# Kernel optimization log

Measured on AMD Instinct MI355X. Metric: run time of the kernel, lower is better.

The kernel has to match this reference:

```python
import jax, jax.numpy as jnp
import numpy as np

N, E, D, H, C = 100000, 1600000, 64, 64, 16


def setup_inputs() -> dict:
    key = jax.random.key(0)
    ks = jax.random.split(key, 8)
    x = jax.random.normal(ks[0], (N, D), dtype=jnp.float32)
    edge_index = jax.random.randint(ks[1], (2, E), 0, N, dtype=jnp.int64)
    W1 = jax.random.normal(ks[2], (D, H), dtype=jnp.float32) * (1.0 / np.sqrt(D))
    b1 = jax.random.normal(ks[3], (H,), dtype=jnp.float32) * 0.01
    W2 = jax.random.normal(ks[4], (H, H), dtype=jnp.float32) * (1.0 / np.sqrt(H))
    b2 = jax.random.normal(ks[5], (H,), dtype=jnp.float32) * 0.01
    Wl = jax.random.normal(ks[6], (H, C), dtype=jnp.float32) * (1.0 / np.sqrt(H))
    bl = jax.random.normal(ks[7], (C,), dtype=jnp.float32) * 0.01
    return {"x": x, "edge_index": edge_index, "W1": W1, "b1": b1,
            "W2": W2, "b2": b2, "Wl": Wl, "bl": bl}


def reference(x, edge_index, W1, b1, W2, b2, Wl, bl):
    n = x.shape[0]
    src, dst = edge_index[0], edge_index[1]
    # GCN symmetric normalization with self-loops: deg = 1 + in-degree at dst
    deg = jax.ops.segment_sum(jnp.ones(src.shape[0], x.dtype), dst, num_segments=n) + 1.0
    inv = jax.lax.rsqrt(deg)                      # deg^{-1/2}, [N]
    norm_e = inv[src] * inv[dst]                  # per-edge norm, [E]
    self_w = inv * inv                            # self-loop weight deg^{-1}, [N]

    def gcn(h, W, b):
        h = h @ W                                 # linear transform first (PyG GCNConv)
        agg = jax.ops.segment_sum(h[src] * norm_e[:, None], dst, num_segments=n)
        agg = agg + h * self_w[:, None]           # self-loop contribution
        return agg + b

    h = jax.nn.relu(gcn(x, W1, b1))
    h = jax.nn.relu(gcn(h, W2, b2))
    return h @ Wl + bl
```

## Files before the change

kernel.cpp:

```cpp
#include <hip/hip_runtime.h>
#include <hip/hip_fp16.h>


#define WS_ALIGN 256
#define BSHIFT 8
#define MAXBUCK 512

typedef _Float16 half8 __attribute__((ext_vector_type(8)));
typedef float floatx4 __attribute__((ext_vector_type(4)));


__global__ void k_bhist(const int* __restrict__ dst, int* __restrict__ bhist,
                        int e, int nbuck) {
    __shared__ int hist[MAXBUCK];
    const int CH = 4096;
    int base = blockIdx.x * CH;
    int end = base + CH; if (end > e) end = e;
    for (int t = threadIdx.x; t < nbuck; t += blockDim.x) hist[t] = 0;
    __syncthreads();
    for (int i = base + threadIdx.x; i < end; i += blockDim.x)
        atomicAdd(&hist[dst[i] >> BSHIFT], 1);
    __syncthreads();
    for (int t = threadIdx.x; t < nbuck; t += blockDim.x)
        if (hist[t]) atomicAdd(&bhist[t], hist[t]);
}

__global__ void k_bscan(const int* __restrict__ bhist, int* __restrict__ gbase,
                        int* __restrict__ gcursor, int e, int nbuck) {
    __shared__ int tmp[MAXBUCK];
    int t = threadIdx.x;
    int v = (t < nbuck) ? bhist[t] : 0;
    tmp[t] = v;
    __syncthreads();
    int x = v;
    #pragma unroll
    for (int d = 1; d < MAXBUCK; d <<= 1) {
        int y = (t >= d) ? tmp[t - d] : 0;
        __syncthreads();
        x += y;
        tmp[t] = x;
        __syncthreads();
    }
    if (t < nbuck) { gbase[t] = x - v; gcursor[t] = x - v; }
    if (t == 0) gbase[nbuck] = e;
}

__global__ void k_partition(const int* __restrict__ src, const int* __restrict__ dst,
                            int* __restrict__ gcursor, int* __restrict__ bpairs,
                            int e, int nbuck) {
    __shared__ int hist[MAXBUCK];
    __shared__ int lbase[MAXBUCK];
    const int CH = 4096;
    int base = blockIdx.x * CH;
    int end = base + CH; if (end > e) end = e;
    for (int t = threadIdx.x; t < nbuck; t += blockDim.x) hist[t] = 0;
    __syncthreads();
    for (int i = base + threadIdx.x; i < end; i += blockDim.x)
        atomicAdd(&hist[dst[i] >> BSHIFT], 1);
    __syncthreads();
    for (int t = threadIdx.x; t < nbuck; t += blockDim.x) {
        int c = hist[t];
        lbase[t] = (c > 0) ? atomicAdd(&gcursor[t], c) : 0;
        hist[t] = 0;
    }
    __syncthreads();
    for (int i = base + threadIdx.x; i < end; i += blockDim.x) {
        int s = src[i], d = dst[i];
        int b = d >> BSHIFT;
        int p = lbase[b] + atomicAdd(&hist[b], 1);
        bpairs[p] = (s << BSHIFT) | (d & ((1 << BSHIFT) - 1));
    }
}

__global__ void k_bfin(const int* __restrict__ bpairs, const int* __restrict__ gbase,
                       int2* __restrict__ ocnt, float* __restrict__ inv,
                       int* __restrict__ ssrc, int n) {
    __shared__ int lcnt[256];
    __shared__ int tmp[256];
    __shared__ int loff[256];
    __shared__ int lcur[256];
    const int b = blockIdx.x;
    const int t = threadIdx.x;
    const int lo = gbase[b];
    const int hi = gbase[b + 1];
    lcnt[t] = 0; lcur[t] = 0;
    __syncthreads();
    for (int i = lo + t; i < hi; i += 256)
        atomicAdd(&lcnt[bpairs[i] & 255], 1);
    __syncthreads();
    int v = lcnt[t];
    tmp[t] = v;
    __syncthreads();
    int x = v;
    #pragma unroll
    for (int d = 1; d < 256; d <<= 1) {
        int y = (t >= d) ? tmp[t - d] : 0;
        __syncthreads();
        x += y;
        tmp[t] = x;
        __syncthreads();
    }
    loff[t] = x - v;
    int node = (b << BSHIFT) + t;
    if (node < n) {
        ocnt[node] = make_int2(lo + (x - v), v);
        inv[node] = rsqrtf((float)v + 1.0f);
    }
    __syncthreads();
    for (int i = lo + t; i < hi; i += 256) {
        int p = bpairs[i];
        int l = p & 255;
        int pos = lo + loff[l] + atomicAdd(&lcur[l], 1);
        ssrc[pos] = p >> BSHIFT;
    }
}


__device__ __forceinline__ void loadA(const float* in, size_t base, half8& a) {
    float4 lo = *reinterpret_cast<const float4*>(in + base);
    float4 hi = *reinterpret_cast<const float4*>(in + base + 16);
    a[0] = (_Float16)lo.x; a[1] = (_Float16)lo.y; a[2] = (_Float16)lo.z; a[3] = (_Float16)lo.w;
    a[4] = (_Float16)hi.x; a[5] = (_Float16)hi.y; a[6] = (_Float16)hi.z; a[7] = (_Float16)hi.w;
}
__device__ __forceinline__ void loadA(const __half* in, size_t base, half8& a) {
    const _Float16* p = reinterpret_cast<const _Float16*>(in + base);
    #pragma unroll
    for (int j = 0; j < 4; ++j) { a[j] = p[j]; a[4 + j] = p[16 + j]; }
}

template <typename Tin>
__global__ void __launch_bounds__(256, 4)
k_transform(const Tin* __restrict__ in, const float* __restrict__ W,
            const float* __restrict__ inv, __half* __restrict__ out, int n) {
    const int lane = threadIdx.x & 63;
    const int m = lane & 15, g = lane >> 4;
    const int wid = blockIdx.x * 4 + (threadIdx.x >> 6);
    const int nw = gridDim.x * 4;

    half8 bf[4][2];
    #pragma unroll
    for (int t = 0; t < 4; ++t)
        #pragma unroll
        for (int s = 0; s < 2; ++s) {
            #pragma unroll
            for (int j = 0; j < 4; ++j) {
                bf[t][s][j]     = (_Float16)W[(32 * s + 4 * g + j) * 64 + 16 * t + m];
                bf[t][s][4 + j] = (_Float16)W[(32 * s + 16 + 4 * g + j) * 64 + 16 * t + m];
            }
        }

    const int ntile = (n + 15) >> 4;
    for (int tile = wid; tile < ntile; tile += nw) {
        const int rbase = tile << 4;
        int arow = rbase + m; if (arow >= n) arow = n - 1;
        half8 a[2];
        loadA(in, (size_t)arow * 64 + 0  + 4 * g, a[0]);
        loadA(in, (size_t)arow * 64 + 32 + 4 * g, a[1]);

        floatx4 acc[4] = {{0.f,0.f,0.f,0.f},{0.f,0.f,0.f,0.f},{0.f,0.f,0.f,0.f},{0.f,0.f,0.f,0.f}};
        #pragma unroll
        for (int s = 0; s < 2; ++s)
            #pragma unroll
            for (int t = 0; t < 4; ++t)
                acc[t] = __builtin_amdgcn_mfma_f32_16x16x32_f16(a[s], bf[t][s], acc[t], 0, 0, 0);

        #pragma unroll
        for (int reg = 0; reg < 4; ++reg) {
            int row = rbase + 4 * g + reg;
            if (row < n) {
                float iv = inv[row];
                #pragma unroll
                for (int t = 0; t < 4; ++t)
                    out[(size_t)row * 64 + 16 * t + m] = __float2half(acc[t][reg] * iv);
            }
        }
    }
}


__global__ void __launch_bounds__(256, 4)
k_aggregate(const __half* __restrict__ t, const int* __restrict__ ssrc,
            const int2* __restrict__ ocnt, const float* __restrict__ inv,
            const float* __restrict__ b, __half* __restrict__ out,
            int n, int do_relu) {
    const int lane = threadIdx.x & 63;
    const int wid = blockIdx.x * (blockDim.x >> 6) + (threadIdx.x >> 6);
    const int nw = gridDim.x * (blockDim.x >> 6);
    const float bj = b[lane];
    for (int node = wid; node < n; node += nw) {
        const int2 oc = ocnt[node];
        const int start = oc.x, cnt = oc.y;
        float acc = 0.f;
        for (int be = 0; be < cnt; be += 64) {
            int m = cnt - be; if (m > 64) m = 64;
            int myidx = (lane < m) ? ssrc[start + be + lane] : 0;
            int j = 0;
            for (; j + 4 <= m; j += 4) {
                int s0 = __builtin_amdgcn_readlane(myidx, j + 0);
                int s1 = __builtin_amdgcn_readlane(myidx, j + 1);
                int s2 = __builtin_amdgcn_readlane(myidx, j + 2);
                int s3 = __builtin_amdgcn_readlane(myidx, j + 3);
                float v0 = __half2float(t[(size_t)s0 * 64 + lane]);
                float v1 = __half2float(t[(size_t)s1 * 64 + lane]);
                float v2 = __half2float(t[(size_t)s2 * 64 + lane]);
                float v3 = __half2float(t[(size_t)s3 * 64 + lane]);
                acc += (v0 + v1) + (v2 + v3);
            }
            for (; j < m; ++j) {
                int s = __builtin_amdgcn_readlane(myidx, j);
                acc += __half2float(t[(size_t)s * 64 + lane]);
            }
        }
        float selfv = __half2float(t[(size_t)node * 64 + lane]);
        float res = fmaf(acc + selfv, inv[node], bj);
        if (do_relu) res = fmaxf(res, 0.f);
        out[(size_t)node * 64 + lane] = __float2half(res);
    }
}


__global__ void k_final(const __half* __restrict__ h, const float* __restrict__ Wl,
                        const float* __restrict__ bl, float* __restrict__ out, int n) {
    __shared__ float Ws[64 * 16];
    for (int i = threadIdx.x; i < 64 * 16; i += blockDim.x) Ws[i] = Wl[i];
    __syncthreads();
    const int lane = threadIdx.x & 63;
    const int r = lane >> 4, c = lane & 15;
    const int wid = blockIdx.x * (blockDim.x >> 6) + (threadIdx.x >> 6);
    const int nw = gridDim.x * (blockDim.x >> 6);
    const float blc = bl[c];
    for (int base = wid * 4; base < n; base += nw * 4) {
        int row = base + r;
        if (row < n) {
            float acc = blc;
            const __half* hrow = h + (size_t)row * 64;
            #pragma unroll
            for (int kk = 0; kk < 8; ++kk) {
                float4 raw = *reinterpret_cast<const float4*>(hrow + kk * 8);
                const __half2* hp = reinterpret_cast<const __half2*>(&raw);
                #pragma unroll
                for (int j = 0; j < 4; ++j) {
                    float2 f = __half22float2(hp[j]);
                    acc = fmaf(f.x, Ws[(kk * 8 + 2 * j + 0) * 16 + c],
                          fmaf(f.y, Ws[(kk * 8 + 2 * j + 1) * 16 + c], acc));
                }
            }
            out[(size_t)row * 16 + c] = acc;
        }
    }
}


extern "C" void kernel_launch(void* const* d_in, const int* in_sizes, int n_in,
                              void* d_out, int out_size, void* d_ws, size_t ws_size,
                              hipStream_t stream) {
    const float* x  = (const float*)d_in[0];
    const int*   ei = (const int*)d_in[1];
    const float* W1 = (const float*)d_in[2];
    const float* b1 = (const float*)d_in[3];
    const float* W2 = (const float*)d_in[4];
    const float* b2 = (const float*)d_in[5];
    const float* Wl = (const float*)d_in[6];
    const float* bl = (const float*)d_in[7];
    float* out = (float*)d_out;

    const int n = in_sizes[0] / 64;
    const int e = in_sizes[1] / 2;
    const int* src = ei;
    const int* dst = ei + e;
    const int nbuck = (n + (1 << BSHIFT) - 1) >> BSHIFT;
    const int nchunk = (e + 4095) / 4096;

    char* ws = (char*)d_ws;
    size_t off = 0;
    auto alloc = [&](size_t bytes) -> void* {
        void* p = ws + off;
        off += (bytes + (WS_ALIGN - 1)) & ~((size_t)WS_ALIGN - 1);
        return p;
    };
    int*    bhist   = (int*)alloc((size_t)MAXBUCK * 4);
    int*    gbase   = (int*)alloc((size_t)(MAXBUCK + 1) * 4);
    int*    gcursor = (int*)alloc((size_t)MAXBUCK * 4);
    int2*   ocnt    = (int2*)alloc((size_t)n * 8);
    float*  inv     = (float*)alloc((size_t)n * 4);
    int*    ssrc    = (int*)alloc((size_t)e * 4);
    __half* bufA    = (__half*)alloc((size_t)n * 64 * 2);
    __half* bufB    = (__half*)alloc((size_t)n * 64 * 2);
    int*    bpairs  = (int*)bufA;

    hipMemsetAsync(bhist, 0, (size_t)MAXBUCK * 4, stream);

    k_bhist<<<nchunk, 256, 0, stream>>>(dst, bhist, e, nbuck);
    k_bscan<<<1, MAXBUCK, 0, stream>>>(bhist, gbase, gcursor, e, nbuck);
    k_partition<<<nchunk, 256, 0, stream>>>(src, dst, gcursor, bpairs, e, nbuck);
    k_bfin<<<nbuck, 256, 0, stream>>>(bpairs, gbase, ocnt, inv, ssrc, n);

    const int ntile = (n + 15) / 16;
    const int tgrid = (ntile + 3) / 4;
    k_transform<float><<<tgrid, 256, 0, stream>>>(x, W1, inv, bufA, n);
    k_aggregate<<<2048, 256, 0, stream>>>(bufA, ssrc, ocnt, inv, b1, bufB, n, 1);
    k_transform<__half><<<tgrid, 256, 0, stream>>>(bufB, W2, inv, bufA, n);
    k_aggregate<<<2048, 256, 0, stream>>>(bufA, ssrc, ocnt, inv, b2, bufB, n, 1);
    k_final<<<2048, 256, 0, stream>>>(bufB, Wl, bl, out, n);
}
```

Before: 195.2 us.

## Gather 8 neighbor rows per wavefront iteration with 16-byte loads in aggregation

The aggregation kernel now splits each wavefront into 8 groups of 8 lanes. Each group loads one full 128-byte fp16 neighbor row as 16-byte vectors, so 8 edges are processed per iteration where the old code did 4 edges with 2-byte loads per lane. Partial sums are reduced across groups with xor shuffles, and the self-loop is folded in as an extra edge. Launch bounds are raised to 8 blocks per SM to increase occupancy. The tradeoff is more registers and shuffle work per node, plus idle lanes when degrees are not multiples of 8.

```diff
diff --git a/kernel.cpp b/kernel.cpp
--- a/kernel.cpp
+++ b/kernel.cpp
@@ -178,43 +178,59 @@
 }
 
 
-__global__ void __launch_bounds__(256, 4)
+__global__ void __launch_bounds__(256, 8)
 k_aggregate(const __half* __restrict__ t, const int* __restrict__ ssrc,
             const int2* __restrict__ ocnt, const float* __restrict__ inv,
             const float* __restrict__ b, __half* __restrict__ out,
             int n, int do_relu) {
     const int lane = threadIdx.x & 63;
+    const int g = lane >> 3;
+    const int f = lane & 7;
     const int wid = blockIdx.x * (blockDim.x >> 6) + (threadIdx.x >> 6);
     const int nw = gridDim.x * (blockDim.x >> 6);
-    const float bj = b[lane];
+    float b8[8];
+    #pragma unroll
+    for (int q = 0; q < 8; ++q) b8[q] = b[f * 8 + q];
+
     for (int node = wid; node < n; node += nw) {
         const int2 oc = ocnt[node];
         const int start = oc.x, cnt = oc.y;
-        float acc = 0.f;
-        for (int be = 0; be < cnt; be += 64) {
-            int m = cnt - be; if (m > 64) m = 64;
-            int myidx = (lane < m) ? ssrc[start + be + lane] : 0;
-            int j = 0;
-            for (; j + 4 <= m; j += 4) {
-                int s0 = __builtin_amdgcn_readlane(myidx, j + 0);
-                int s1 = __builtin_amdgcn_readlane(myidx, j + 1);
-                int s2 = __builtin_amdgcn_readlane(myidx, j + 2);
-                int s3 = __builtin_amdgcn_readlane(myidx, j + 3);
-                float v0 = __half2float(t[(size_t)s0 * 64 + lane]);
-                float v1 = __half2float(t[(size_t)s1 * 64 + lane]);
-                float v2 = __half2float(t[(size_t)s2 * 64 + lane]);
-                float v3 = __half2float(t[(size_t)s3 * 64 + lane]);
-                acc += (v0 + v1) + (v2 + v3);
-            }
-            for (; j < m; ++j) {
-                int s = __builtin_amdgcn_readlane(myidx, j);
-                acc += __half2float(t[(size_t)s * 64 + lane]);
-            }
-        }
-        float selfv = __half2float(t[(size_t)node * 64 + lane]);
-        float res = fmaf(acc + selfv, inv[node], bj);
-        if (do_relu) res = fmaxf(res, 0.f);
-        out[(size_t)node * 64 + lane] = __float2half(res);
+        const int tot = cnt + 1;
+        float acc[8] = {0.f,0.f,0.f,0.f,0.f,0.f,0.f,0.f};
+        for (int be = 0; be < tot; be += 64) {
+            int lim = tot - be; if (lim > 64) lim = 64;
+            int myidx = (be + lane < cnt) ? ssrc[start + be + lane] : node;
+            for (int j = 0; j < lim; j += 8) {
+                int epos = j + g;
+                int sidx = __shfl(myidx, epos);
+                float wt = (epos < lim) ? 1.f : 0.f;
+                float4 raw = *reinterpret_cast<const float4*>(t + (size_t)sidx * 64 + f * 8);
+                const __half2* hp = reinterpret_cast<const __half2*>(&raw);
+                #pragma unroll
+                for (int q = 0; q < 4; ++q) {
+                    float2 fv = __half22float2(hp[q]);
+                    acc[2 * q]     = fmaf(fv.x, wt, acc[2 * q]);
+                    acc[2 * q + 1] = fmaf(fv.y, wt, acc[2 * q + 1]);
+                }
+            }
+        }
+        #pragma unroll
+        for (int off = 8; off < 64; off <<= 1)
+            #pragma unroll
+            for (int q = 0; q < 8; ++q)
+                acc[q] += __shfl_xor(acc[q], off);
+        if (g == 0) {
+            const float iv = inv[node];
+            __half hres[8];
+            #pragma unroll
+            for (int q = 0; q < 8; ++q) {
+                float r = fmaf(acc[q], iv, b8[q]);
+                if (do_relu) r = fmaxf(r, 0.f);
+                hres[q] = __float2half(r);
+            }
+            *reinterpret_cast<float4*>(out + (size_t)node * 64 + f * 8) =
+                *reinterpret_cast<const float4*>(hres);
+        }
     }
 }
 
@@ -240,9 +256,9 @@
                 const __half2* hp = reinterpret_cast<const __half2*>(&raw);
                 #pragma unroll
                 for (int j = 0; j < 4; ++j) {
-                    float2 f = __half22float2(hp[j]);
-                    acc = fmaf(f.x, Ws[(kk * 8 + 2 * j + 0) * 16 + c],
-                          fmaf(f.y, Ws[(kk * 8 + 2 * j + 1) * 16 + c], acc));
+                    float2 fv = __half22float2(hp[j]);
+                    acc = fmaf(fv.x, Ws[(kk * 8 + 2 * j + 0) * 16 + c],
+                          fmaf(fv.y, Ws[(kk * 8 + 2 * j + 1) * 16 + c], acc));
                 }
             }
             out[(size_t)row * 16 + c] = acc;
```

Result: faster. 181.8 us (-6.9%).
